# Performance work log

Measured on AMD Instinct MI355X. Metric: run time of the kernel, lower is better.

The kernel has to match this reference:

```python
import jax, jax.numpy as jnp
import numpy as np
import math

N = 768      # N_res
CS = 384     # c_s
CZ = 128     # c_z
CH = 16      # c_hidden
H = 12       # num_heads
PQK = 4      # num_qk_points
PV = 8       # num_v_points
INF = 100000.0
EPS = 1e-8
SOFTPLUS_INV_1 = 0.541324854612918


def setup_inputs() -> dict:
    key = jax.random.key(0)
    ks = jax.random.split(key, 16)
    rn = lambda k, sh, sc=1.0: jax.random.normal(k, sh, dtype=jnp.float32) * sc
    s = rn(ks[0], (N, CS))
    z = rn(ks[1], (N, N, CZ))
    mask = jnp.ones((N,), jnp.float32)
    rot, _ = jnp.linalg.qr(rn(ks[2], (N, 3, 3)))  # proper orthonormal frames
    rot = rot.astype(jnp.float32)
    trans = rn(ks[3], (N, 3))
    sc = 0.02
    w_q = rn(ks[4], (CS, H * CH), sc)
    w_k = rn(ks[5], (CS, H * CH), sc)
    w_v = rn(ks[6], (CS, H * CH), sc)
    w_qp = rn(ks[7], (CS, H * 3 * PQK), sc)
    b_qp = jnp.zeros((H * 3 * PQK,), jnp.float32)
    w_kp = rn(ks[8], (CS, H * 3 * PQK), sc)
    b_kp = jnp.zeros((H * 3 * PQK,), jnp.float32)
    w_vp = rn(ks[9], (CS, H * 3 * PV), sc)
    b_vp = jnp.zeros((H * 3 * PV,), jnp.float32)
    w_b = rn(ks[10], (CZ, H), sc)
    b_b = jnp.zeros((H,), jnp.float32)
    head_weights = jnp.full((H,), SOFTPLUS_INV_1, jnp.float32)
    cat_dim = H * (CZ + CH + 4 * PV)  # 2112
    w_out = rn(ks[11], (cat_dim, CS), sc)
    b_out = jnp.zeros((CS,), jnp.float32)
    return dict(s=s, z=z, mask=mask, rot=rot, trans=trans,
                w_q=w_q, w_k=w_k, w_v=w_v,
                w_qp=w_qp, b_qp=b_qp, w_kp=w_kp, b_kp=b_kp,
                w_vp=w_vp, b_vp=b_vp, w_b=w_b, b_b=b_b,
                head_weights=head_weights, w_out=w_out, b_out=b_out)


def _project_points(x, w, b, rot, trans, n_pts):
    # torch layout: linear -> [N, H, 3*P]; split into 3 chunks of P (x,y,z); stack dim=-1
    pl = (x @ w + b).reshape(N, H, 3, n_pts)
    pl = jnp.swapaxes(pl, -1, -2)  # [N, H, P, 3]
    # rigid apply: R @ p + t
    return jnp.einsum('nij,nhpj->nhpi', rot, pl) + trans[:, None, None, :]


def reference(s, z, mask, rot, trans, w_q, w_k, w_v, w_qp, b_qp, w_kp, b_kp,
              w_vp, b_vp, w_b, b_b, head_weights, w_out, b_out):
    # point attention weights
    pw = math.sqrt(2.0 / (9.0 * max(PQK, 1)))
    hw = jnp.logaddexp(head_weights, 0.0)  # softplus
    point_weights = pw * hw  # [H]

    q_pts = _project_points(s, w_qp, b_qp, rot, trans, PQK)  # [N,H,Pqk,3]
    k_pts = _project_points(s, w_kp, b_kp, rot, trans, PQK)

    # sum_p |q - k|^2 expanded to avoid the [N,N,H,P,3] intermediate
    sq_q = jnp.sum(q_pts * q_pts, axis=(-1, -2))  # [N,H]
    sq_k = jnp.sum(k_pts * k_pts, axis=(-1, -2))  # [N,H]
    cross = jnp.einsum('qhpd,khpd->qkh', q_pts, k_pts)
    d2 = sq_q[:, None, :] + sq_k[None, :, :] - 2.0 * cross  # [N,N,H]
    pt_att = (-0.5) * d2 * point_weights  # broadcast over h

    # scalar QK attention
    scalar_w = math.sqrt(1.0 / max(CH, 1))
    q = (s @ w_q).reshape(N, H, CH) * scalar_w
    k = (s @ w_k).reshape(N, H, CH)
    qk = jnp.einsum('qhc,khc->qkh', q, k)

    # pair bias
    b_bias = z @ w_b + b_b  # [N,N,H]

    sq_mask = mask[:, None] * mask[None, :]  # [N,N]
    mask_bias = INF * (sq_mask - 1.0)

    logits = (pt_att + qk + b_bias + mask_bias[..., None]) * math.sqrt(1.0 / 3.0)
    a = jax.nn.softmax(logits, axis=-2)  # softmax over key dim, [N,N,H]

    # scalar values
    v = (s @ w_v).reshape(N, H, CH)
    o = jnp.einsum('qkh,khc->qhc', a, v).reshape(N, H * CH)

    # point values
    v_pts = _project_points(s, w_vp, b_vp, rot, trans, PV)  # [N,H,Pv,3]
    o_pt = jnp.einsum('qkh,khpd->qhpd', a, v_pts).reshape(N, H * PV, 3)
    # back to local frame: R^T (p - t)
    o_pt_local = jnp.einsum('nji,nmj->nmi', rot, o_pt - trans[:, None, :])  # [N,H*Pv,3]
    norm2 = jnp.sum(o_pt_local * o_pt_local, axis=-1)
    o_pt_norm = jnp.sqrt(jnp.maximum(norm2, EPS * EPS))  # [N,H*Pv]

    # pair output
    o_pair = jnp.einsum('qkh,qkc->qhc', a, z).reshape(N, H * CZ)

    cat = jnp.concatenate(
        [o, o_pt_local[..., 0], o_pt_local[..., 1], o_pt_local[..., 2],
         o_pt_norm, o_pair], axis=-1)  # [N, H*(c_z+c_hidden+4*Pv)]
    return cat @ w_out + b_out  # [N, c_s]
```

## Files before the change

kernel.cpp:

```cpp
#include <hip/hip_runtime.h>
#include <hip/hip_bf16.h>
#include <math.h>

#define NRES 768
#define CS 384
#define CZ 128
#define NH 12
#define INF_ 100000.0f
#define CAT 2112
#define LQ 776

typedef __attribute__((ext_vector_type(8))) short bf16x8;
typedef __attribute__((ext_vector_type(4))) float f32x4;

#define WS_Q      0
#define WS_K      147456
#define WS_QPL    294912
#define WS_KPL    405504
#define WS_VPL    516096
#define WS_QPT    737280
#define WS_KPT    847872
#define WS_SQQ    958464
#define WS_SQK    967680
#define WS_VCAT   976896
#define WS_CAT    1345536

__device__ __forceinline__ short f2bf(float f) {
  union { float f; unsigned u; } x; x.f = f;
  unsigned r = x.u + 0x7FFFu + ((x.u >> 16) & 1u);
  return (short)(r >> 16);
}

__device__ __forceinline__ f32x4 mfma16(bf16x8 a, bf16x8 b, f32x4 c) {
  return __builtin_amdgcn_mfma_f32_16x16x32_bf16(a, b, c, 0, 0, 0);
}

__device__ __forceinline__ bf16x8 pack8(const float* p) {
  float4 a0 = *(const float4*)p;
  float4 a1 = *(const float4*)(p + 4);
  bf16x8 v;
  v[0] = f2bf(a0.x); v[1] = f2bf(a0.y); v[2] = f2bf(a0.z); v[3] = f2bf(a0.w);
  v[4] = f2bf(a1.x); v[5] = f2bf(a1.y); v[6] = f2bf(a1.z); v[7] = f2bf(a1.w);
  return v;
}

__global__ __launch_bounds__(256) void k_proj(
    const float* __restrict__ s,
    const float* __restrict__ w_q, const float* __restrict__ w_k, const float* __restrict__ w_v,
    const float* __restrict__ w_qp, const float* __restrict__ b_qp,
    const float* __restrict__ w_kp, const float* __restrict__ b_kp,
    const float* __restrict__ w_vp, const float* __restrict__ b_vp,
    float* __restrict__ ws)
{
  int mt = blockIdx.x;
  int wv = threadIdx.x >> 6;
  int lane = threadIdx.x & 63;
  int nt = blockIdx.y * 4 + wv;
  const float* W; const float* B = nullptr; int OC, j0, seg;
  if (nt < 12)      { W = w_q;  OC = 192; j0 = nt*16;       seg = 0; }
  else if (nt < 24) { W = w_k;  OC = 192; j0 = nt*16 - 192; seg = 1; }
  else if (nt < 36) { W = w_v;  OC = 192; j0 = nt*16 - 384; seg = 2; }
  else if (nt < 45) { W = w_qp; OC = 144; j0 = nt*16 - 576; seg = 3; B = b_qp; }
  else if (nt < 54) { W = w_kp; OC = 144; j0 = nt*16 - 720; seg = 4; B = b_kp; }
  else              { W = w_vp; OC = 288; j0 = nt*16 - 864; seg = 5; B = b_vp; }
  int col = lane & 15, g = lane >> 4;
  f32x4 acc = {0.f, 0.f, 0.f, 0.f};
  for (int ks = 0; ks < 12; ks++) {
    bf16x8 av = pack8(s + (size_t)(mt*16 + col)*CS + ks*32 + g*8);
    const float* bp = W + (size_t)(ks*32 + g*8)*OC + j0 + col;
    bf16x8 bv;
    #pragma unroll
    for (int j = 0; j < 8; j++) bv[j] = f2bf(bp[(size_t)j*OC]);
    acc = mfma16(av, bv, acc);
  }
  float bias = B ? B[j0 + col] : 0.f;
  float* q_ws = ws + WS_Q;  float* k_ws = ws + WS_K;
  float* qpl  = ws + WS_QPL; float* kpl = ws + WS_KPL; float* vpl = ws + WS_VPL;
  float* vcat = ws + WS_VCAT;
  int jc = j0 + col;
  #pragma unroll
  for (int r = 0; r < 4; r++) {
    int n = mt*16 + g*4 + r;
    float v = acc[r] + bias;
    switch (seg) {
      case 0: q_ws[n*192 + jc] = v * 0.25f; break;
      case 1: k_ws[n*192 + jc] = v; break;
      case 2: vcat[n*480 + jc] = v; break;
      case 3: qpl[n*144 + jc] = v; break;
      case 4: kpl[n*144 + jc] = v; break;
      default: vpl[n*288 + jc] = v; break;
    }
  }
}

__global__ __launch_bounds__(192) void k_rigid(
    const float* __restrict__ rot, const float* __restrict__ trans, float* __restrict__ ws)
{
  int n = blockIdx.x; int t = threadIdx.x;
  __shared__ float sq[96];
  const float* R = rot + n*9; const float* T = trans + n*3;
  float R00=R[0],R01=R[1],R02=R[2],R10=R[3],R11=R[4],R12=R[5],R20=R[6],R21=R[7],R22=R[8];
  float T0=T[0],T1=T[1],T2=T[2];
  if (t < 96) {
    int isK = (t >= 48); int m = isK ? t - 48 : t;
    int h = m >> 2, p = m & 3;
    const float* L = ws + (isK ? WS_KPL : WS_QPL) + n*144 + h*12;
    float px = L[p], py = L[4 + p], pz = L[8 + p];
    float gx = R00*px + R01*py + R02*pz + T0;
    float gy = R10*px + R11*py + R12*pz + T1;
    float gz = R20*px + R21*py + R22*pz + T2;
    float* O = ws + (isK ? WS_KPT : WS_QPT) + n*144 + h*12 + p*3;
    O[0] = gx; O[1] = gy; O[2] = gz;
    sq[t] = gx*gx + gy*gy + gz*gz;
  } else {
    int m = t - 96; int h = m >> 3, p = m & 7;
    const float* L = ws + WS_VPL + n*288 + h*24;
    float px = L[p], py = L[8 + p], pz = L[16 + p];
    float gx = R00*px + R01*py + R02*pz + T0;
    float gy = R10*px + R11*py + R12*pz + T1;
    float gz = R20*px + R21*py + R22*pz + T2;
    float* O = ws + WS_VCAT + n*480 + 192 + h*24 + p*3;
    O[0] = gx; O[1] = gy; O[2] = gz;
  }
  __syncthreads();
  if (t < 12) {
    ws[WS_SQQ + n*12 + t] = sq[t*4] + sq[t*4+1] + sq[t*4+2] + sq[t*4+3];
  } else if (t < 24) {
    int h = t - 12;
    ws[WS_SQK + n*12 + h] = sq[48+h*4] + sq[48+h*4+1] + sq[48+h*4+2] + sq[48+h*4+3];
  }
}

__global__ __launch_bounds__(512) void k_attn(
    const float* __restrict__ z, const float* __restrict__ mask,
    const float* __restrict__ w_b, const float* __restrict__ b_b,
    const float* __restrict__ head_weights,
    const float* __restrict__ rot, const float* __restrict__ trans,
    float* __restrict__ ws)
{
  int q = blockIdx.x; int tid = threadIdx.x;
  int lane = tid & 63; int wv = tid >> 6;
  int colh = lane & 15, g = lane >> 4;
  __shared__ float s_logits[NH * LQ];
  __shared__ short s_abf[16 * LQ];
  __shared__ float s_qv[192], s_qp[144], s_sqq[12], s_pw[12], s_bb[12];
  __shared__ float s_opt[288];
  const float* k_ws = ws + WS_K;
  const float* k_pts = ws + WS_KPT;
  const float* sq_k = ws + WS_SQK;
  const float* vcat = ws + WS_VCAT;
  float* cat = ws + WS_CAT;

  if (tid < 192) s_qv[tid] = ws[WS_Q + q*192 + tid];
  else if (tid < 336) s_qp[tid-192] = ws[WS_QPT + q*144 + (tid-192)];
  else if (tid < 348) s_sqq[tid-336] = ws[WS_SQQ + q*12 + (tid-336)];
  else if (tid < 360) {
    int h = tid - 348; float x = head_weights[h];
    float sp = fmaxf(x, 0.f) + log1pf(__expf(-fabsf(x)));
    s_pw[h] = 0.23570226039551584f * sp;
  }
  else if (tid < 372) s_bb[tid-360] = b_b[tid-360];
  for (int i = tid; i < 4*LQ; i += 512) s_abf[12*LQ + i] = 0;
  __syncthreads();

  float maskq = mask[q];
  for (int i = tid; i < NRES*NH; i += 512) {
    int kk = i / 12, h = i % 12;
    const float* kv = k_ws + kk*192 + h*16;
    const float* qv = s_qv + h*16;
    float qk = 0.f;
    #pragma unroll
    for (int c = 0; c < 16; c++) qk += kv[c]*qv[c];
    const float* kp = k_pts + kk*144 + h*12;
    const float* qp = s_qp + h*12;
    float cr = 0.f;
    #pragma unroll
    for (int j = 0; j < 12; j++) cr += kp[j]*qp[j];
    float d2 = s_sqq[h] + sq_k[kk*12 + h] - 2.f*cr;
    float v = qk - 0.5f*s_pw[h]*d2 + s_bb[h] + INF_*(maskq*mask[kk] - 1.f);
    s_logits[h*LQ + kk] = v;
  }
  __syncthreads();

  bf16x8 wbf[4];
  #pragma unroll
  for (int ks = 0; ks < 4; ks++) {
    #pragma unroll
    for (int j = 0; j < 8; j++) {
      int c = ks*32 + g*8 + j;
      wbf[ks][j] = (colh < 12) ? f2bf(w_b[c*12 + colh]) : (short)0;
    }
  }
  for (int mtile = wv; mtile < 48; mtile += 8) {
    int k0 = mtile * 16;
    f32x4 acc = {0.f, 0.f, 0.f, 0.f};
    #pragma unroll
    for (int ks = 0; ks < 4; ks++) {
      bf16x8 av = pack8(z + ((size_t)q*NRES + k0 + colh)*CZ + ks*32 + g*8);
      acc = mfma16(av, wbf[ks], acc);
    }
    if (colh < 12) {
      #pragma unroll
      for (int r = 0; r < 4; r++)
        s_logits[colh*LQ + k0 + g*4 + r] += acc[r];
    }
  }
  __syncthreads();

  for (int h = wv; h < NH; h += 8) {
    float v[12]; float m = -1e30f;
    #pragma unroll
    for (int i = 0; i < 12; i++) {
      v[i] = s_logits[h*LQ + lane + i*64] * 0.57735026919f;
      m = fmaxf(m, v[i]);
    }
    #pragma unroll
    for (int d = 1; d < 64; d <<= 1) m = fmaxf(m, __shfl_xor(m, d));
    float sum = 0.f;
    #pragma unroll
    for (int i = 0; i < 12; i++) { v[i] = __expf(v[i] - m); sum += v[i]; }
    #pragma unroll
    for (int d = 1; d < 64; d <<= 1) sum += __shfl_xor(sum, d);
    float inv = 1.f / sum;
    #pragma unroll
    for (int i = 0; i < 12; i++) {
      float p = v[i] * inv;
      s_logits[h*LQ + lane + i*64] = p;
      s_abf[h*LQ + lane + i*64] = f2bf(p);
    }
  }
  __syncthreads();

  {
    int c0 = wv * 16;
    f32x4 acc = {0.f, 0.f, 0.f, 0.f};
    for (int ks = 0; ks < 24; ks++) {
      bf16x8 av = *(const bf16x8*)&s_abf[colh*LQ + ks*32 + g*8];
      const float* bp = z + ((size_t)q*NRES + ks*32 + g*8)*CZ + c0 + colh;
      bf16x8 bv;
      #pragma unroll
      for (int j = 0; j < 8; j++) bv[j] = f2bf(bp[(size_t)j*CZ]);
      acc = mfma16(av, bv, acc);
    }
    #pragma unroll
    for (int r = 0; r < 4; r++) {
      int hh = g*4 + r;
      if (hh < 12) cat[(size_t)q*CAT + 576 + hh*128 + c0 + colh] = acc[r];
    }
  }

  if (tid < 480) {
    int oi = tid;
    int h = (oi < 192) ? (oi >> 4) : ((oi - 192) / 24);
    float acc = 0.f;
    #pragma unroll 4
    for (int k = 0; k < NRES; k += 4) {
      float4 p4 = *(const float4*)&s_logits[h*LQ + k];
      const float* vp = vcat + (size_t)k*480 + oi;
      acc += p4.x*vp[0] + p4.y*vp[480] + p4.z*vp[960] + p4.w*vp[1440];
    }
    if (oi < 192) cat[(size_t)q*CAT + oi] = acc;
    else s_opt[oi - 192] = acc;
  }
  __syncthreads();

  if (tid < 96) {
    int m = tid;
    float x = s_opt[m*3], y = s_opt[m*3+1], zz = s_opt[m*3+2];
    const float* R = rot + q*9; const float* T = trans + q*3;
    float dx = x - T[0], dy = y - T[1], dz = zz - T[2];
    float lx = R[0]*dx + R[3]*dy + R[6]*dz;
    float ly = R[1]*dx + R[4]*dy + R[7]*dz;
    float lz = R[2]*dx + R[5]*dy + R[8]*dz;
    float n2 = lx*lx + ly*ly + lz*lz;
    cat[(size_t)q*CAT + 192 + m] = lx;
    cat[(size_t)q*CAT + 288 + m] = ly;
    cat[(size_t)q*CAT + 384 + m] = lz;
    cat[(size_t)q*CAT + 480 + m] = sqrtf(fmaxf(n2, 1e-16f));
  }
}

__global__ __launch_bounds__(256) void k_out(
    const float* __restrict__ ws, const float* __restrict__ w_out,
    const float* __restrict__ b_out, float* __restrict__ out)
{
  const float* cat = ws + WS_CAT;
  int mt = blockIdx.x;
  int wv = threadIdx.x >> 6, lane = threadIdx.x & 63;
  int nt = blockIdx.y*4 + wv;
  int col = lane & 15, g = lane >> 4;
  float bias = b_out[nt*16 + col];
  f32x4 acc = {bias, bias, bias, bias};
  for (int ks = 0; ks < 66; ks++) {
    bf16x8 av = pack8(cat + (size_t)(mt*16 + col)*CAT + ks*32 + g*8);
    const float* bp = w_out + (size_t)(ks*32 + g*8)*CS + nt*16 + col;
    bf16x8 bv;
    #pragma unroll
    for (int j = 0; j < 8; j++) bv[j] = f2bf(bp[(size_t)j*CS]);
    acc = mfma16(av, bv, acc);
  }
  #pragma unroll
  for (int r = 0; r < 4; r++)
    out[(size_t)(mt*16 + g*4 + r)*CS + nt*16 + col] = acc[r];
}

extern "C" void kernel_launch(void* const* d_in, const int* in_sizes, int n_in,
                              void* d_out, int out_size, void* d_ws, size_t ws_size,
                              hipStream_t stream) {
  const float* s     = (const float*)d_in[0];
  const float* z     = (const float*)d_in[1];
  const float* mask  = (const float*)d_in[2];
  const float* rot   = (const float*)d_in[3];
  const float* trans = (const float*)d_in[4];
  const float* w_q   = (const float*)d_in[5];
  const float* w_k   = (const float*)d_in[6];
  const float* w_v   = (const float*)d_in[7];
  const float* w_qp  = (const float*)d_in[8];
  const float* b_qp  = (const float*)d_in[9];
  const float* w_kp  = (const float*)d_in[10];
  const float* b_kp  = (const float*)d_in[11];
  const float* w_vp  = (const float*)d_in[12];
  const float* b_vp  = (const float*)d_in[13];
  const float* w_b   = (const float*)d_in[14];
  const float* b_b   = (const float*)d_in[15];
  const float* hw    = (const float*)d_in[16];
  const float* w_out = (const float*)d_in[17];
  const float* b_out = (const float*)d_in[18];
  float* out = (float*)d_out;
  float* ws  = (float*)d_ws;

  k_proj <<<dim3(48, 18), 256, 0, stream>>>(s, w_q, w_k, w_v, w_qp, b_qp, w_kp, b_kp, w_vp, b_vp, ws);
  k_rigid<<<768, 192, 0, stream>>>(rot, trans, ws);
  k_attn <<<768, 512, 0, stream>>>(z, mask, w_b, b_b, hw, rot, trans, ws);
  k_out  <<<dim3(48, 6), 256, 0, stream>>>(ws, w_out, b_out, out);
}
```

Baseline: 650.5 us.

## Alias bf16 attention probabilities onto logits LDS with XOR swizzle to raise occupancy

Drops the separate bf16 probability buffer and writes the bf16 softmax output into the same shared memory as the fp32 logits, using an XOR-swizzled layout to avoid bank conflicts on the MFMA A-operand reads. Softmax is restructured so each wave handles one head, then four waves handle the rest after a barrier. The value/point accumulation now reads bf16 probabilities instead of fp32. Launch bounds request 6 blocks per CU. Together these cut LDS use so more blocks fit per CU, at the cost of lower precision in the scalar and point value sums.

```diff
diff --git a/kernel.cpp b/kernel.cpp
--- a/kernel.cpp
+++ b/kernel.cpp
@@ -8,10 +8,12 @@
 #define NH 12
 #define INF_ 100000.0f
 #define CAT 2112
-#define LQ 776
+#define LQF 775
 
 typedef __attribute__((ext_vector_type(8))) short bf16x8;
 typedef __attribute__((ext_vector_type(4))) float f32x4;
+
+#define ABF(row,k) ((row)*768 + ((k) ^ (((row)&7)<<3)))
 
 #define WS_Q      0
 #define WS_K      147456
@@ -29,6 +31,12 @@
   union { float f; unsigned u; } x; x.f = f;
   unsigned r = x.u + 0x7FFFu + ((x.u >> 16) & 1u);
   return (short)(r >> 16);
+}
+
+__device__ __forceinline__ float bf2f(short s) {
+  union { unsigned u; float f; } t;
+  t.u = ((unsigned)(unsigned short)s) << 16;
+  return t.f;
 }
 
 __device__ __forceinline__ f32x4 mfma16(bf16x8 a, bf16x8 b, f32x4 c) {
@@ -131,7 +139,7 @@
   }
 }
 
-__global__ __launch_bounds__(512) void k_attn(
+__global__ __launch_bounds__(512, 6) void k_attn(
     const float* __restrict__ z, const float* __restrict__ mask,
     const float* __restrict__ w_b, const float* __restrict__ b_b,
     const float* __restrict__ head_weights,
@@ -141,8 +149,8 @@
   int q = blockIdx.x; int tid = threadIdx.x;
   int lane = tid & 63; int wv = tid >> 6;
   int colh = lane & 15, g = lane >> 4;
-  __shared__ float s_logits[NH * LQ];
-  __shared__ short s_abf[16 * LQ];
+  __shared__ float s_logits[NH * LQF];
+  short* s_abf = (short*)s_logits;
   __shared__ float s_qv[192], s_qp[144], s_sqq[12], s_pw[12], s_bb[12];
   __shared__ float s_opt[288];
   const float* k_ws = ws + WS_K;
@@ -160,7 +168,6 @@
     s_pw[h] = 0.23570226039551584f * sp;
   }
   else if (tid < 372) s_bb[tid-360] = b_b[tid-360];
-  for (int i = tid; i < 4*LQ; i += 512) s_abf[12*LQ + i] = 0;
   __syncthreads();
 
   float maskq = mask[q];
@@ -178,7 +185,7 @@
     for (int j = 0; j < 12; j++) cr += kp[j]*qp[j];
     float d2 = s_sqq[h] + sq_k[kk*12 + h] - 2.f*cr;
     float v = qk - 0.5f*s_pw[h]*d2 + s_bb[h] + INF_*(maskq*mask[kk] - 1.f);
-    s_logits[h*LQ + kk] = v;
+    s_logits[h*LQF + kk] = v;
   }
   __syncthreads();
 
@@ -202,16 +209,16 @@
     if (colh < 12) {
       #pragma unroll
       for (int r = 0; r < 4; r++)
-        s_logits[colh*LQ + k0 + g*4 + r] += acc[r];
-    }
-  }
-  __syncthreads();
-
-  for (int h = wv; h < NH; h += 8) {
+        s_logits[colh*LQF + k0 + g*4 + r] += acc[r];
+    }
+  }
+  __syncthreads();
+
+  {
     float v[12]; float m = -1e30f;
     #pragma unroll
     for (int i = 0; i < 12; i++) {
-      v[i] = s_logits[h*LQ + lane + i*64] * 0.57735026919f;
+      v[i] = s_logits[wv*LQF + lane + i*64] * 0.57735026919f;
       m = fmaxf(m, v[i]);
     }
     #pragma unroll
@@ -222,11 +229,34 @@
     #pragma unroll
     for (int d = 1; d < 64; d <<= 1) sum += __shfl_xor(sum, d);
     float inv = 1.f / sum;
-    #pragma unroll
-    for (int i = 0; i < 12; i++) {
-      float p = v[i] * inv;
-      s_logits[h*LQ + lane + i*64] = p;
-      s_abf[h*LQ + lane + i*64] = f2bf(p);
+    __syncthreads();
+    #pragma unroll
+    for (int i = 0; i < 12; i++)
+      s_abf[ABF(wv, lane + i*64)] = f2bf(v[i] * inv);
+    if (wv < 4) {
+      int h = wv + 8;
+      float w[12]; float m2 = -1e30f;
+      #pragma unroll
+      for (int i = 0; i < 12; i++) {
+        w[i] = s_logits[h*LQF + lane + i*64] * 0.57735026919f;
+        m2 = fmaxf(m2, w[i]);
+      }
+      #pragma unroll
+      for (int d = 1; d < 64; d <<= 1) m2 = fmaxf(m2, __shfl_xor(m2, d));
+      float sum2 = 0.f;
+      #pragma unroll
+      for (int i = 0; i < 12; i++) { w[i] = __expf(w[i] - m2); sum2 += w[i]; }
+      #pragma unroll
+      for (int d = 1; d < 64; d <<= 1) sum2 += __shfl_xor(sum2, d);
+      float inv2 = 1.f / sum2;
+      #pragma unroll
+      for (int i = 0; i < 12; i++)
+        s_abf[ABF(h, lane + i*64)] = f2bf(w[i] * inv2);
+    } else {
+      int h = wv + 8;
+      #pragma unroll
+      for (int i = 0; i < 12; i++)
+        s_abf[ABF(h, lane + i*64)] = 0;
     }
   }
   __syncthreads();
@@ -235,7 +265,7 @@
     int c0 = wv * 16;
     f32x4 acc = {0.f, 0.f, 0.f, 0.f};
     for (int ks = 0; ks < 24; ks++) {
-      bf16x8 av = *(const bf16x8*)&s_abf[colh*LQ + ks*32 + g*8];
+      bf16x8 av = *(const bf16x8*)&s_abf[ABF(colh, ks*32 + g*8)];
       const float* bp = z + ((size_t)q*NRES + ks*32 + g*8)*CZ + c0 + colh;
       bf16x8 bv;
       #pragma unroll
@@ -253,11 +283,12 @@
     int oi = tid;
     int h = (oi < 192) ? (oi >> 4) : ((oi - 192) / 24);
     float acc = 0.f;
-    #pragma unroll 4
-    for (int k = 0; k < NRES; k += 4) {
-      float4 p4 = *(const float4*)&s_logits[h*LQ + k];
-      const float* vp = vcat + (size_t)k*480 + oi;
-      acc += p4.x*vp[0] + p4.y*vp[480] + p4.z*vp[960] + p4.w*vp[1440];
+    for (int k0 = 0; k0 < NRES; k0 += 8) {
+      bf16x8 pv = *(const bf16x8*)&s_abf[ABF(h, k0)];
+      const float* vp = vcat + (size_t)k0*480 + oi;
+      #pragma unroll
+      for (int j = 0; j < 8; j++)
+        acc += bf2f(pv[j]) * vp[(size_t)j*480];
     }
     if (oi < 192) cat[(size_t)q*CAT + oi] = acc;
     else s_opt[oi - 192] = acc;
```

Result: faster. 608.9 us (-6.4%).
